# Kernel optimization log

Measured on AMD Instinct MI355X. Metric: run time of the kernel, lower is better.

## Reference

```python
import math
import jax, jax.numpy as jnp
import numpy as np

B, TQ, TK, D = 2, 512, 8192, 1024
N_HEAD, HEAD_DIM = 16, 64
NA = 4096


def setup_inputs() -> dict:
    key = jax.random.key(0)
    ks = jax.random.split(key, 12)
    w = lambda k, shp: (jax.random.normal(k, shp, dtype=jnp.float32) * 0.02)
    return {
        "q": jax.random.normal(ks[0], (B, TQ, D), dtype=jnp.float32),
        "kv": jax.random.normal(ks[1], (B, TK, D), dtype=jnp.float32),
        "Wq": w(ks[2], (D, D)), "bq": jnp.zeros((D,), jnp.float32),
        "Wk": w(ks[3], (D, D)), "bk": jnp.zeros((D,), jnp.float32),
        "Wv": w(ks[4], (D, D)), "bv": jnp.zeros((D,), jnp.float32),
        "Wo": w(ks[5], (D, D)), "bo": jnp.zeros((D,), jnp.float32),
        "active_bias": w(ks[6], (1, D)),
        "inactive_bias": w(ks[7], (1, D)),
        "log_temp": jnp.zeros((), jnp.float32),  # log(temp=1.0)
        "n_actives": NA,
    }


def _attn(qh, kh, vh):
    # qh already carries the full score scale; plain softmax attention
    scores = jnp.einsum("bhqd,bhkd->bhqk", qh, kh)
    w = jax.nn.softmax(scores, axis=-1)
    return jnp.einsum("bhqk,bhkd->bhqd", w, vh)


def reference(q, kv, Wq, bq, Wk, bk, Wv, bv, Wo, bo, active_bias, inactive_bias, log_temp, n_actives):
    Na = int(n_actives)
    Tk = kv.shape[1]
    Ni = Tk - Na

    qp = jnp.einsum("btd,od->bto", q, Wq) + bq
    # group-specific additive biases on kv before K/V projection
    kvb = jnp.concatenate([kv[:, :Na] + active_bias, kv[:, Na:] + inactive_bias], axis=1)
    kp = jnp.einsum("btd,od->bto", kvb, Wk) + bk
    vp = jnp.einsum("btd,od->bto", kvb, Wv) + bv

    # [B, H, T, hd]
    qh = qp.reshape(B, TQ, N_HEAD, HEAD_DIM).transpose(0, 2, 1, 3)
    kh = kp.reshape(B, Tk, N_HEAD, HEAD_DIM).transpose(0, 2, 1, 3)
    vh = vp.reshape(B, Tk, N_HEAD, HEAD_DIM).transpose(0, 2, 1, 3)

    temp = jnp.clip(jnp.exp(log_temp), 0.1, 10.0)
    # torch: q *= 1/sqrt(d); sdpa(q/temp, ...) applies another 1/sqrt(d)
    qs = qh / (jnp.float32(HEAD_DIM) * temp)

    out = jnp.zeros_like(qh)
    if Na > 0:
        out = out + _attn(qs, kh[:, :, :Na], vh[:, :, :Na]) / math.sqrt(max(Na, 1))
    if Ni > 0:
        out = out - _attn(qs, kh[:, :, Na:], vh[:, :, Na:]) / math.sqrt(max(Ni, 1))

    out = out.transpose(0, 2, 1, 3).reshape(B, TQ, D)
    return jnp.einsum("btd,od->bto", out, Wo) + bo
```

## Files before the change

kernel.cpp:

```cpp
#include <hip/hip_runtime.h>
#include <math.h>
#include <stdint.h>

#define B_   2
#define TQ_  512
#define TK_  8192
#define D_   1024
#define NH_  16
#define HD_  64

#define NEG_BIG (-3.0e38f)
#define ASPLIT 8
#define LOG2E 1.4426950408889634f
#define EXP2F(x) __builtin_exp2f(x)

typedef __attribute__((ext_vector_type(8))) short short8;
typedef __attribute__((ext_vector_type(4))) float f32x4;

__device__ __forceinline__ unsigned short f2bf(float x) {
    unsigned u = __float_as_uint(x);
    unsigned r = u + 0x7FFFu + ((u >> 16) & 1u);
    return (unsigned short)(r >> 16);
}
__device__ __forceinline__ float bf2f(unsigned short h) {
    return __uint_as_float(((unsigned)h) << 16);
}
__device__ __forceinline__ short8 pack_bf16x8(float4 lo, float4 hi) {
    union { short8 v; unsigned u[4]; } P;
    asm("v_cvt_pk_bf16_f32 %0, %1, %2" : "=v"(P.u[0]) : "v"(lo.x), "v"(lo.y));
    asm("v_cvt_pk_bf16_f32 %0, %1, %2" : "=v"(P.u[1]) : "v"(lo.z), "v"(lo.w));
    asm("v_cvt_pk_bf16_f32 %0, %1, %2" : "=v"(P.u[2]) : "v"(hi.x), "v"(hi.y));
    asm("v_cvt_pk_bf16_f32 %0, %1, %2" : "=v"(P.u[3]) : "v"(hi.z), "v"(hi.w));
    return P.v;
}

#define GLD16(gp, lp)                                                              \
    __builtin_amdgcn_global_load_lds(                                              \
        (const __attribute__((address_space(1))) unsigned int*)(gp),               \
        (__attribute__((address_space(3))) unsigned int*)(lp), 16, 0, 0)

__global__ __launch_bounds__(256)
void split_w4(const float* __restrict__ W0, const float* __restrict__ W1,
              const float* __restrict__ W2, const float* __restrict__ W3,
              unsigned short* __restrict__ O0, unsigned short* __restrict__ O1,
              unsigned short* __restrict__ O2, unsigned short* __restrict__ O3)
{
    const float* W; unsigned short* O;
    switch (blockIdx.y) {
        case 0:  W = W0; O = O0; break;
        case 1:  W = W1; O = O1; break;
        case 2:  W = W2; O = O2; break;
        default: W = W3; O = O3; break;
    }
    size_t i = ((size_t)blockIdx.x * 256 + threadIdx.x) * 8;
    float4 x0 = *(const float4*)(W + i);
    float4 x1 = *(const float4*)(W + i + 4);
    float a[8] = {x0.x, x0.y, x0.z, x0.w, x1.x, x1.y, x1.z, x1.w};
    union { short8 v; unsigned short u[8]; } H;
#pragma unroll
    for (int j = 0; j < 8; ++j) H.u[j] = f2bf(a[j]);
    *(short8*)(O + i) = H.v;
}

__global__ __launch_bounds__(256)
void split_w(const float* __restrict__ W, unsigned short* __restrict__ Wh)
{
    size_t i = ((size_t)blockIdx.x * 256 + threadIdx.x) * 8;
    float4 x0 = *(const float4*)(W + i);
    float4 x1 = *(const float4*)(W + i + 4);
    float a[8] = {x0.x, x0.y, x0.z, x0.w, x1.x, x1.y, x1.z, x1.w};
    union { short8 v; unsigned short u[8]; } H;
#pragma unroll
    for (int j = 0; j < 8; ++j) H.u[j] = f2bf(a[j]);
    *(short8*)(Wh + i) = H.v;
}

__global__ __launch_bounds__(256)
void bias_gemv(const float* __restrict__ Wk, const float* __restrict__ Wv,
               const float* __restrict__ ab, const float* __restrict__ ib,
               float* __restrict__ gvK, float* __restrict__ gvV)
{
    const int comb = blockIdx.y;
    const float* W = (comb < 2) ? Wk : Wv;
    const float* g = (comb & 1) ? ib : ab;
    float* out = ((comb < 2) ? gvK : gvV) + (comb & 1) * D_;
    const int n = blockIdx.x * 256 + threadIdx.x;
    const float* wr = W + (size_t)n * D_;
    float acc = 0.f;
    for (int d = 0; d < D_; d += 4) {
        float4 w4 = *(const float4*)(wr + d);
        float4 g4 = *(const float4*)(g + d);
        acc += w4.x * g4.x + w4.y * g4.y + w4.z * g4.z + w4.w * g4.w;
    }
    out[n] = acc;
}

__global__ __launch_bounds__(256)
void sdpca_gemm_q(const unsigned short* __restrict__ A, const unsigned short* __restrict__ W,
                  const float* __restrict__ bias, const float* __restrict__ log_temp,
                  unsigned short* __restrict__ Qb)
{
    __shared__ unsigned short AT[128 * 32];
    __shared__ unsigned short BT[128 * 32];
    const int tid  = threadIdx.x;
    const int lane = tid & 63;
    const int w    = tid >> 6;
    const int brow = blockIdx.y * 128;
    const int bcol = blockIdx.x * 128;
    const int wr = w >> 1, wc = w & 1;

    const int   srow = lane >> 2;
    const int   scol = (((lane & 3) ^ ((lane >> 3) & 3)) * 8);
    const size_t gA0 = (size_t)(brow + w * 32 + srow) * D_ + scol;
    const size_t gA1 = gA0 + (size_t)16 * D_;
    const size_t gB0 = (size_t)(bcol + w * 32 + srow) * D_ + scol;
    const size_t gB1 = gB0 + (size_t)16 * D_;
    const int   l0   = (w * 32 +  0) * 32;
    const int   l1   = (w * 32 + 16) * 32;

    f32x4 acc[4][4];
#pragma unroll
    for (int m = 0; m < 4; ++m)
#pragma unroll
        for (int n = 0; n < 4; ++n) acc[m][n] = (f32x4){0.f, 0.f, 0.f, 0.f};

    const int frow = lane & 15;
    const int fko  = (((lane >> 4) ^ ((frow >> 1) & 3)) * 8);

    for (int k0 = 0; k0 < D_; k0 += 32) {
        GLD16(A + gA0 + k0, &AT[l0]);
        GLD16(A + gA1 + k0, &AT[l1]);
        GLD16(W + gB0 + k0, &BT[l0]);
        GLD16(W + gB1 + k0, &BT[l1]);
        __syncthreads();
        short8 bf[4];
#pragma unroll
        for (int n = 0; n < 4; ++n)
            bf[n] = *(const short8*)&BT[(wc * 64 + n * 16 + frow) * 32 + fko];
#pragma unroll
        for (int m = 0; m < 4; ++m) {
            short8 a = *(const short8*)&AT[(wr * 64 + m * 16 + frow) * 32 + fko];
#pragma unroll
            for (int n = 0; n < 4; ++n)
                acc[m][n] = __builtin_amdgcn_mfma_f32_16x16x32_bf16(a, bf[n], acc[m][n], 0, 0, 0);
        }
        __syncthreads();
    }

    float lt    = *log_temp;
    float temp  = fminf(fmaxf(expf(lt), 0.1f), 10.0f);
    float scale = LOG2E / (64.0f * temp);

#pragma unroll
    for (int n = 0; n < 4; ++n) {
        int col = bcol + wc * 64 + n * 16 + frow;
        float bsv = bias[col];
#pragma unroll
        for (int m = 0; m < 4; ++m) {
            int rbase = brow + wr * 64 + m * 16 + (lane >> 4) * 4;
#pragma unroll
            for (int r = 0; r < 4; ++r)
                Qb[(size_t)(rbase + r) * D_ + col] = f2bf((acc[m][n][r] + bsv) * scale);
        }
    }
}

__global__ __launch_bounds__(256)
void sdpca_gemm_kv_fused(const float* __restrict__ kv,
                         const unsigned short* __restrict__ Whk,
                         const unsigned short* __restrict__ Whv,
                         const float* __restrict__ bk, const float* __restrict__ bv,
                         const float* __restrict__ gvK, const float* __restrict__ gvV,
                         const int* __restrict__ nactp,
                         unsigned short* __restrict__ Kb, unsigned short* __restrict__ Vt)
{
    __shared__ unsigned short AT[128 * 32];
    __shared__ unsigned short BT[128 * 32];

    const int tid  = threadIdx.x;
    const int lane = tid & 63;
    const int w    = tid >> 6;
    const int bid  = blockIdx.x;
    const int lid  = (bid & 7) * 128 + (bid >> 3);
    const int brow = (lid >> 3) * 128;
    const int bcol = (lid & 7) * 128;
    const int z    = blockIdx.y;
    const int Na   = *nactp;

    const unsigned short* Wh = z ? Whv : Whk;
    const float* bias        = z ? bv  : bk;
    const float* gv          = z ? gvV : gvK;

    const int wr = w >> 1, wc = w & 1;

    const int srow = lane >> 2;
    const int cg   = lane & 3;
    const int cs   = cg ^ ((srow >> 1) & 3);
    const size_t gA0 = (size_t)(brow + w * 32 + srow) * D_ + cg * 8;
    const size_t gA1 = gA0 + (size_t)16 * D_;
    const size_t gB0 = (size_t)(bcol + w * 32 + srow) * D_ + cg * 8;
    const size_t gB1 = gB0 + (size_t)16 * D_;
    const int    la0 = (w * 32 + srow) * 32 + cs * 8;
    const int    la1 = (w * 32 + 16 + srow) * 32 + cs * 8;

    f32x4 acc[4][4];
#pragma unroll
    for (int m = 0; m < 4; ++m)
#pragma unroll
        for (int n = 0; n < 4; ++n) acc[m][n] = (f32x4){0.f, 0.f, 0.f, 0.f};

    const int frow = lane & 15;
    const int fko  = (((lane >> 4) ^ ((frow >> 1) & 3)) * 8);

    float4 a00 = *(const float4*)(kv + gA0);
    float4 a01 = *(const float4*)(kv + gA0 + 4);
    float4 a10 = *(const float4*)(kv + gA1);
    float4 a11 = *(const float4*)(kv + gA1 + 4);
    short8 br0 = *(const short8*)(Wh + gB0);
    short8 br1 = *(const short8*)(Wh + gB1);

    for (int k0 = 0; k0 < D_; k0 += 32) {
        __syncthreads();
        *(short8*)&AT[la0] = pack_bf16x8(a00, a01);
        *(short8*)&AT[la1] = pack_bf16x8(a10, a11);
        *(short8*)&BT[la0] = br0;
        *(short8*)&BT[la1] = br1;
        __syncthreads();

        if (k0 + 32 < D_) {
            a00 = *(const float4*)(kv + gA0 + k0 + 36 - 4);
            a01 = *(const float4*)(kv + gA0 + k0 + 36);
            a10 = *(const float4*)(kv + gA1 + k0 + 32);
            a11 = *(const float4*)(kv + gA1 + k0 + 36);
            br0 = *(const short8*)(Wh + gB0 + k0 + 32);
            br1 = *(const short8*)(Wh + gB1 + k0 + 32);
        }

        short8 bf[4];
#pragma unroll
        for (int n = 0; n < 4; ++n)
            bf[n] = *(const short8*)&BT[(wc * 64 + n * 16 + frow) * 32 + fko];
#pragma unroll
        for (int m = 0; m < 4; ++m) {
            short8 a = *(const short8*)&AT[(wr * 64 + m * 16 + frow) * 32 + fko];
#pragma unroll
            for (int n = 0; n < 4; ++n)
                acc[m][n] = __builtin_amdgcn_mfma_f32_16x16x32_bf16(a, bf[n], acc[m][n], 0, 0, 0);
        }
    }

    if (z == 0) {
#pragma unroll
        for (int n = 0; n < 4; ++n) {
            int col = bcol + wc * 64 + n * 16 + frow;
            float bsv = bias[col];
            float g0  = gv[col], g1 = gv[D_ + col];
#pragma unroll
            for (int m = 0; m < 4; ++m) {
                int rbase = brow + wr * 64 + m * 16 + (lane >> 4) * 4;
#pragma unroll
                for (int r = 0; r < 4; ++r) {
                    int tok = (rbase + r) & (TK_ - 1);
                    float gval = (tok < Na) ? g0 : g1;
                    Kb[(size_t)(rbase + r) * D_ + col] = f2bf(acc[m][n][r] + bsv + gval);
                }
            }
        }
    } else {
#pragma unroll
        for (int n = 0; n < 4; ++n) {
            int col = bcol + wc * 64 + n * 16 + frow;
            int h   = col >> 6, d = col & 63;
            float bsv = bias[col];
            float g0  = gv[col], g1 = gv[D_ + col];
#pragma unroll
            for (int m = 0; m < 4; ++m) {
                int rbase = brow + wr * 64 + m * 16 + (lane >> 4) * 4;
                int b     = rbase >> 13;
                int tok   = rbase & (TK_ - 1);
                ushort4 o;
                o.x = f2bf(acc[m][n][0] + bsv + ((tok + 0 < Na) ? g0 : g1));
                o.y = f2bf(acc[m][n][1] + bsv + ((tok + 1 < Na) ? g0 : g1));
                o.z = f2bf(acc[m][n][2] + bsv + ((tok + 2 < Na) ? g0 : g1));
                o.w = f2bf(acc[m][n][3] + bsv + ((tok + 3 < Na) ? g0 : g1));
                *(ushort4*)&Vt[((size_t)(b * 16 + h) * 64 + d) * TK_ + tok] = o;
            }
        }
    }
}

template<bool FULL>
__device__ __forceinline__ void attn_pass(
    const f32x4 st[4], int jb, int lo, int hi,
    f32x4& lacc, f32x4 o[4],
    unsigned short* Ps, const unsigned short* Vs,
    int frow, int g, int w)
{
    const int q = w * 16 + frow;
    const short8 kOnes = {(short)0x3F80, (short)0x3F80, (short)0x3F80, (short)0x3F80,
                          (short)0x3F80, (short)0x3F80, (short)0x3F80, (short)0x3F80};
    float p[4][4];
#pragma unroll
    for (int mt = 0; mt < 4; ++mt)
#pragma unroll
        for (int r = 0; r < 4; ++r) {
            float pv = EXP2F(st[mt][r]);
            if (!FULL) {
                int key = jb + mt * 16 + g * 4 + r;
                if (key < lo || key >= hi) pv = 0.f;
            }
            p[mt][r] = pv;
        }

#pragma unroll
    for (int mt = 0; mt < 4; ++mt) {
        unsigned u0, u1;
        asm("v_cvt_pk_bf16_f32 %0, %1, %2" : "=v"(u0) : "v"(p[mt][0]), "v"(p[mt][1]));
        asm("v_cvt_pk_bf16_f32 %0, %1, %2" : "=v"(u1) : "v"(p[mt][2]), "v"(p[mt][3]));
        unsigned* dst = (unsigned*)((char*)Ps + q * 144 + (mt * 16 + g * 4) * 2);
        dst[0] = u0; dst[1] = u1;
    }
    __builtin_amdgcn_sched_barrier(0);

    short8 pb[2];
#pragma unroll
    for (int ks = 0; ks < 2; ++ks)
        pb[ks] = *(const short8*)((const char*)Ps + q * 144 + ks * 64 + g * 16);
    __builtin_amdgcn_s_setprio(1);
#pragma unroll
    for (int mt = 0; mt < 4; ++mt) {
        int row = mt * 16 + frow;
        int rs  = (row & 7) << 4;
#pragma unroll
        for (int ks = 0; ks < 2; ++ks) {
            short8 a = *(const short8*)((const char*)Vs + row * 128 + ((ks * 64 + g * 16) ^ rs));
            o[mt] = __builtin_amdgcn_mfma_f32_16x16x32_bf16(a, pb[ks], o[mt], 0, 0, 0);
        }
    }
#pragma unroll
    for (int ks = 0; ks < 2; ++ks)
        lacc = __builtin_amdgcn_mfma_f32_16x16x32_bf16(kOnes, pb[ks], lacc, 0, 0, 0);
    __builtin_amdgcn_s_setprio(0);
}

__global__ __launch_bounds__(256)
void sdpca_attn_mfma(const unsigned short* __restrict__ Qb,
                     const unsigned short* __restrict__ Kb,
                     const unsigned short* __restrict__ Vt,
                     const int* __restrict__ nactp,
                     unsigned short* __restrict__ pO, float* __restrict__ pL)
{
    __shared__ char smem[25600];
    unsigned short* Ks = (unsigned short*)smem;
    unsigned short* Vs = (unsigned short*)(smem + 8192);
    unsigned short* Ps = (unsigned short*)(smem + 16384);
    float*          Ot = (float*)smem;

    const int tid  = threadIdx.x;
    const int l    = tid & 63, w = tid >> 6;
    const int frow = l & 15,  g = l >> 4;

    const int bid = blockIdx.x;
    const int lid = (bid & 7) * 256 + (bid >> 3);
    const int q0  = (lid & 7) * 64;
    const int bh  = (lid >> 3) & 31;
    const int s   = lid >> 8;
    const int b   = bh >> 4, h = bh & 15;

    const int Na   = *nactp;
    const int ks0  = s * (TK_ / ASPLIT);
    const int nt   = TK_ / ASPLIT / 64;

    short8 qf0, qf1;
    {
        const unsigned short* qp = Qb + (size_t)(b * TQ_ + q0 + w * 16 + frow) * D_ + h * HD_;
        qf0 = *(const short8*)(qp + g * 8);
        qf1 = *(const short8*)(qp + 32 + g * 8);
    }

    f32x4 lA4 = (f32x4){0.f, 0.f, 0.f, 0.f};
    f32x4 lI4 = (f32x4){0.f, 0.f, 0.f, 0.f};
    f32x4 oA[4], oI[4];
#pragma unroll
    for (int mt = 0; mt < 4; ++mt) {
        oA[mt] = (f32x4){0.f, 0.f, 0.f, 0.f};
        oI[mt] = (f32x4){0.f, 0.f, 0.f, 0.f};
    }

    const int srow = tid >> 2;
    const int scb  = (tid & 3) * 32;
    const unsigned short* kg = Kb + (size_t)(b * TK_ + ks0 + srow) * D_ + h * HD_ + (tid & 3) * 16;
    const unsigned short* vg = Vt + ((size_t)bh * HD_ + srow) * TK_ + ks0 + (tid & 3) * 16;
    const int kswz0 = srow * 128 + ((scb +  0) ^ ((srow & 7) << 4));
    const int kswz1 = srow * 128 + ((scb + 16) ^ ((srow & 7) << 4));

    short8 kr0 = *(const short8*)(kg);
    short8 kr1 = *(const short8*)(kg + 8);
    short8 vr0 = *(const short8*)(vg);
    short8 vr1 = *(const short8*)(vg + 8);
    kg += (size_t)64 * D_;
    vg += 64;

    for (int t = 0; t < nt; ++t) {
        const int jb = ks0 + t * 64;
        __syncthreads();
        *(short8*)((char*)Ks + kswz0) = kr0;
        *(short8*)((char*)Ks + kswz1) = kr1;
        *(short8*)((char*)Vs + kswz0) = vr0;
        *(short8*)((char*)Vs + kswz1) = vr1;
        __syncthreads();

        if (t + 1 < nt) {
            kr0 = *(const short8*)(kg);
            kr1 = *(const short8*)(kg + 8);
            vr0 = *(const short8*)(vg);
            vr1 = *(const short8*)(vg + 8);
            kg += (size_t)64 * D_;
            vg += 64;
        }

        f32x4 st[4];
        __builtin_amdgcn_s_setprio(1);
#pragma unroll
        for (int mt = 0; mt < 4; ++mt) {
            int row = mt * 16 + frow;
            int rs  = (row & 7) << 4;
            short8 a0 = *(const short8*)((const char*)Ks + row * 128 + ((g * 16) ^ rs));
            short8 a1 = *(const short8*)((const char*)Ks + row * 128 + ((64 + g * 16) ^ rs));
            f32x4 acc = (f32x4){0.f, 0.f, 0.f, 0.f};
            acc = __builtin_amdgcn_mfma_f32_16x16x32_bf16(a0, qf0, acc, 0, 0, 0);
            acc = __builtin_amdgcn_mfma_f32_16x16x32_bf16(a1, qf1, acc, 0, 0, 0);
            st[mt] = acc;
        }
        __builtin_amdgcn_s_setprio(0);

        const bool hasA = (jb < Na);
        const bool hasI = (jb + 64 > Na);
        if (hasA) {
            if (jb + 64 <= Na) attn_pass<true >(st, jb, 0, Na, lA4, oA, Ps, Vs, frow, g, w);
            else               attn_pass<false>(st, jb, 0, Na, lA4, oA, Ps, Vs, frow, g, w);
        }
        if (hasI) {
            if (jb >= Na)      attn_pass<true >(st, jb, Na, TK_, lI4, oI, Ps, Vs, frow, g, w);
            else               attn_pass<false>(st, jb, Na, TK_, lI4, oI, Ps, Vs, frow, g, w);
        }
    }

    const int q = w * 16 + frow;
#pragma unroll
    for (int grp = 0; grp < 2; ++grp) {
        __syncthreads();
        const f32x4* o = grp ? oI : oA;
#pragma unroll
        for (int mt = 0; mt < 4; ++mt)
            *(f32x4*)&Ot[q * 68 + mt * 16 + g * 4] = o[mt];
        if (g == 0) {
            size_t base = ((size_t)((s * 2 + grp) * (B_ * NH_) + bh)) * TQ_ + q0 + q;
            pL[base] = grp ? lI4[0] : lA4[0];
        }
        __syncthreads();
        {
            int qr = tid >> 2, dc = (tid & 3) * 16;
            size_t rowbase = ((size_t)((s * 2 + grp) * (B_ * NH_) + bh)) * TQ_ + q0 + qr;
            unsigned short* dst = pO + rowbase * HD_ + dc;
            union { short8 v; unsigned short u[8]; } o0, o1;
#pragma unroll
            for (int j = 0; j < 8; ++j) {
                o0.u[j] = f2bf(Ot[qr * 68 + dc + j]);
                o1.u[j] = f2bf(Ot[qr * 68 + dc + 8 + j]);
            }
            *(short8*)(dst)     = o0.v;
            *(short8*)(dst + 8) = o1.v;
        }
    }
}

__global__ __launch_bounds__(256)
void sdpca_combine(const unsigned short* __restrict__ pO, const float* __restrict__ pL,
                   const int* __restrict__ nactp, unsigned short* __restrict__ Aob)
{
    int idx = blockIdx.x * 256 + threadIdx.x;
    int d   = idx & (HD_ - 1);
    int q   = (idx >> 6) & (TQ_ - 1);
    int bh  = idx >> 15;
    int b   = bh >> 4, h = bh & 15;
    int Na  = *nactp;
    int Ni  = TK_ - Na;

    float res = 0.f;
#pragma unroll
    for (int gg = 0; gg < 2; ++gg) {
        float L = 0.f, O = 0.f;
#pragma unroll
        for (int ss = 0; ss < ASPLIT; ++ss) {
            size_t ii = ((size_t)((ss * 2 + gg) * (B_ * NH_) + bh)) * TQ_ + q;
            L += pL[ii];
            O += bf2f(pO[ii * HD_ + d]);
        }
        float r   = (L > 0.f) ? (O / L) : 0.f;
        int   cnt = (gg == 0) ? Na : Ni;
        float sc  = (cnt > 0) ? rsqrtf((float)cnt) : 0.f;
        res += (gg == 0) ? (sc * r) : (-sc * r);
    }
    Aob[((size_t)(b * TQ_ + q)) * D_ + h * HD_ + d] = f2bf(res);
}

__global__ __launch_bounds__(256)
void sdpca_gemm_o(const unsigned short* __restrict__ A, const unsigned short* __restrict__ W,
                  const float* __restrict__ bias, float* __restrict__ C)
{
    __shared__ unsigned short AT[128 * 32];
    __shared__ unsigned short BT[128 * 32];
    const int tid  = threadIdx.x;
    const int lane = tid & 63;
    const int w    = tid >> 6;
    const int brow = blockIdx.y * 128;
    const int bcol = blockIdx.x * 128;
    const int wr = w >> 1, wc = w & 1;

    const int   srow = lane >> 2;
    const int   scol = (((lane & 3) ^ ((lane >> 3) & 3)) * 8);
    const size_t gA0 = (size_t)(brow + w * 32 + srow) * D_ + scol;
    const size_t gA1 = gA0 + (size_t)16 * D_;
    const size_t gB0 = (size_t)(bcol + w * 32 + srow) * D_ + scol;
    const size_t gB1 = gB0 + (size_t)16 * D_;
    const int   l0   = (w * 32 +  0) * 32;
    const int   l1   = (w * 32 + 16) * 32;

    f32x4 acc[4][4];
#pragma unroll
    for (int m = 0; m < 4; ++m)
#pragma unroll
        for (int n = 0; n < 4; ++n) acc[m][n] = (f32x4){0.f, 0.f, 0.f, 0.f};

    const int frow = lane & 15;
    const int fko  = (((lane >> 4) ^ ((frow >> 1) & 3)) * 8);

    for (int k0 = 0; k0 < D_; k0 += 32) {
        GLD16(A + gA0 + k0, &AT[l0]);
        GLD16(A + gA1 + k0, &AT[l1]);
        GLD16(W + gB0 + k0, &BT[l0]);
        GLD16(W + gB1 + k0, &BT[l1]);
        __syncthreads();
        short8 bf[4];
#pragma unroll
        for (int n = 0; n < 4; ++n)
            bf[n] = *(const short8*)&BT[(wc * 64 + n * 16 + frow) * 32 + fko];
#pragma unroll
        for (int m = 0; m < 4; ++m) {
            short8 a = *(const short8*)&AT[(wr * 64 + m * 16 + frow) * 32 + fko];
#pragma unroll
            for (int n = 0; n < 4; ++n)
                acc[m][n] = __builtin_amdgcn_mfma_f32_16x16x32_bf16(a, bf[n], acc[m][n], 0, 0, 0);
        }
        __syncthreads();
    }

#pragma unroll
    for (int n = 0; n < 4; ++n) {
        int col = bcol + wc * 64 + n * 16 + frow;
        float bsv = bias[col];
#pragma unroll
        for (int m = 0; m < 4; ++m) {
            int rbase = brow + wr * 64 + m * 16 + (lane >> 4) * 4;
#pragma unroll
            for (int r = 0; r < 4; ++r)
                C[(size_t)(rbase + r) * D_ + col] = acc[m][n][r] + bsv;
        }
    }
}

extern "C" void kernel_launch(void* const* d_in, const int* in_sizes, int n_in,
                              void* d_out, int out_size, void* d_ws, size_t ws_size,
                              hipStream_t stream) {
    (void)in_sizes; (void)n_in; (void)out_size; (void)ws_size;
    const float* q   = (const float*)d_in[0];
    const float* kv  = (const float*)d_in[1];
    const float* Wq  = (const float*)d_in[2];
    const float* bq  = (const float*)d_in[3];
    const float* Wk  = (const float*)d_in[4];
    const float* bk  = (const float*)d_in[5];
    const float* Wv  = (const float*)d_in[6];
    const float* bv  = (const float*)d_in[7];
    const float* Wo  = (const float*)d_in[8];
    const float* bo  = (const float*)d_in[9];
    const float* ab  = (const float*)d_in[10];
    const float* ib  = (const float*)d_in[11];
    const float* lt  = (const float*)d_in[12];
    const int*   na  = (const int*)d_in[13];

    char* ws = (char*)d_ws;
    const size_t nQ  = (size_t)B_ * TQ_ * D_;
    const size_t nKV = (size_t)B_ * TK_ * D_;
    const size_t nW  = (size_t)D_ * D_;
    const size_t nML = (size_t)ASPLIT * 2 * B_ * NH_ * TQ_;

    float*          gvK = (float*)ws;
    float*          gvV = gvK + 2 * D_;
    unsigned short* Whk = (unsigned short*)(gvV + 2 * D_);
    unsigned short* Whv = Whk + nW;
    unsigned short* Kb  = Whv + nW;
    unsigned short* Vt  = Kb + nKV;
    unsigned short* Qb  = Vt + nKV;
    unsigned short* qbb = Qb + nQ;
    unsigned short* Wqb = qbb + nQ;
    unsigned short* Wob = Wqb + nW;
    unsigned short* Aob = Wob + nW;
    float* pL = (float*)(Aob + nQ);
    unsigned short* pO = (unsigned short*)(pL + nML);

    dim3 blk(256);
    split_w            <<<dim3((int)(nQ / 8 / 256)),  blk, 0, stream>>>(q,  qbb);
    split_w4           <<<dim3((int)(nW / 8 / 256), 4), blk, 0, stream>>>(
        Wq, Wo, Wk, Wv, Wqb, Wob, Whk, Whv);
    bias_gemv          <<<dim3(4, 4),                 blk, 0, stream>>>(Wk, Wv, ab, ib, gvK, gvV);
    sdpca_gemm_q       <<<dim3(8, 8),                 blk, 0, stream>>>(qbb, Wqb, bq, lt, Qb);
    sdpca_gemm_kv_fused<<<dim3(1024, 2),              blk, 0, stream>>>(
        kv, Whk, Whv, bk, bv, gvK, gvV, na, Kb, Vt);
    sdpca_attn_mfma    <<<dim3(2048),                 blk, 0, stream>>>(Qb, Kb, Vt, na, pO, pL);
    sdpca_combine      <<<dim3((B_ * TQ_ * D_) / 256), blk, 0, stream>>>(pO, pL, na, Aob);
    sdpca_gemm_o       <<<dim3(8, 8),                 blk, 0, stream>>>(Aob, Wob, bo, (float*)d_out);
}
```

Baseline: 257.1 us.

## Stream fp32 kv tiles directly to LDS and merge q cast into weight split

The KV projection GEMM now loads fp32 kv tiles straight into shared memory with global_load_lds using an XOR-swizzled layout, converting to bf16 only when forming MFMA fragments. The weight tiles are also loaded via global_load_lds, replacing the register prefetch plus LDS store path. The separate q-to-bf16 cast kernel is folded into the weight split kernel as a fifth grid slice, which works because nQ equals nW here. In exchange the fp32 A tile doubles LDS use, there is no register-level prefetch overlap, and every wave repeats the bf16 pack work inside the inner loop.

```diff
diff --git a/kernel.cpp b/kernel.cpp
--- a/kernel.cpp
+++ b/kernel.cpp
@@ -25,12 +25,12 @@
 __device__ __forceinline__ float bf2f(unsigned short h) {
     return __uint_as_float(((unsigned)h) << 16);
 }
-__device__ __forceinline__ short8 pack_bf16x8(float4 lo, float4 hi) {
+__device__ __forceinline__ short8 pack_bf16x8(f32x4 lo, f32x4 hi) {
     union { short8 v; unsigned u[4]; } P;
-    asm("v_cvt_pk_bf16_f32 %0, %1, %2" : "=v"(P.u[0]) : "v"(lo.x), "v"(lo.y));
-    asm("v_cvt_pk_bf16_f32 %0, %1, %2" : "=v"(P.u[1]) : "v"(lo.z), "v"(lo.w));
-    asm("v_cvt_pk_bf16_f32 %0, %1, %2" : "=v"(P.u[2]) : "v"(hi.x), "v"(hi.y));
-    asm("v_cvt_pk_bf16_f32 %0, %1, %2" : "=v"(P.u[3]) : "v"(hi.z), "v"(hi.w));
+    asm("v_cvt_pk_bf16_f32 %0, %1, %2" : "=v"(P.u[0]) : "v"(lo[0]), "v"(lo[1]));
+    asm("v_cvt_pk_bf16_f32 %0, %1, %2" : "=v"(P.u[1]) : "v"(lo[2]), "v"(lo[3]));
+    asm("v_cvt_pk_bf16_f32 %0, %1, %2" : "=v"(P.u[2]) : "v"(hi[0]), "v"(hi[1]));
+    asm("v_cvt_pk_bf16_f32 %0, %1, %2" : "=v"(P.u[3]) : "v"(hi[2]), "v"(hi[3]));
     return P.v;
 }
 
@@ -40,17 +40,20 @@
         (__attribute__((address_space(3))) unsigned int*)(lp), 16, 0, 0)
 
 __global__ __launch_bounds__(256)
-void split_w4(const float* __restrict__ W0, const float* __restrict__ W1,
+void split_w5(const float* __restrict__ W0, const float* __restrict__ W1,
               const float* __restrict__ W2, const float* __restrict__ W3,
+              const float* __restrict__ W4,
               unsigned short* __restrict__ O0, unsigned short* __restrict__ O1,
-              unsigned short* __restrict__ O2, unsigned short* __restrict__ O3)
+              unsigned short* __restrict__ O2, unsigned short* __restrict__ O3,
+              unsigned short* __restrict__ O4)
 {
     const float* W; unsigned short* O;
     switch (blockIdx.y) {
         case 0:  W = W0; O = O0; break;
         case 1:  W = W1; O = O1; break;
         case 2:  W = W2; O = O2; break;
-        default: W = W3; O = O3; break;
+        case 3:  W = W3; O = O3; break;
+        default: W = W4; O = O4; break;
     }
     size_t i = ((size_t)blockIdx.x * 256 + threadIdx.x) * 8;
     float4 x0 = *(const float4*)(W + i);
@@ -60,19 +63,6 @@
 #pragma unroll
     for (int j = 0; j < 8; ++j) H.u[j] = f2bf(a[j]);
     *(short8*)(O + i) = H.v;
-}
-
-__global__ __launch_bounds__(256)
-void split_w(const float* __restrict__ W, unsigned short* __restrict__ Wh)
-{
-    size_t i = ((size_t)blockIdx.x * 256 + threadIdx.x) * 8;
-    float4 x0 = *(const float4*)(W + i);
-    float4 x1 = *(const float4*)(W + i + 4);
-    float a[8] = {x0.x, x0.y, x0.z, x0.w, x1.x, x1.y, x1.z, x1.w};
-    union { short8 v; unsigned short u[8]; } H;
-#pragma unroll
-    for (int j = 0; j < 8; ++j) H.u[j] = f2bf(a[j]);
-    *(short8*)(Wh + i) = H.v;
 }
 
 __global__ __launch_bounds__(256)
@@ -174,8 +164,8 @@
                          const int* __restrict__ nactp,
                          unsigned short* __restrict__ Kb, unsigned short* __restrict__ Vt)
 {
-    __shared__ unsigned short AT[128 * 32];
-    __shared__ unsigned short BT[128 * 32];
+    __shared__ float          ATf[128 * 32];
+    __shared__ unsigned short BT [128 * 32];
 
     const int tid  = threadIdx.x;
     const int lane = tid & 63;
@@ -193,15 +183,16 @@
 
     const int wr = w >> 1, wc = w & 1;
 
-    const int srow = lane >> 2;
-    const int cg   = lane & 3;
-    const int cs   = cg ^ ((srow >> 1) & 3);
-    const size_t gA0 = (size_t)(brow + w * 32 + srow) * D_ + cg * 8;
-    const size_t gA1 = gA0 + (size_t)16 * D_;
-    const size_t gB0 = (size_t)(bcol + w * 32 + srow) * D_ + cg * 8;
-    const size_t gB1 = gB0 + (size_t)16 * D_;
-    const int    la0 = (w * 32 + srow) * 32 + cs * 8;
-    const int    la1 = (w * 32 + 16 + srow) * 32 + cs * 8;
+    const int    arow = lane >> 3;
+    const int    acs  = (lane & 7) ^ arow;
+    const size_t gAr  = (size_t)(brow + w * 32 + arow) * D_ + acs * 4;
+
+    const int    srow = lane >> 2;
+    const int    scol = (((lane & 3) ^ ((lane >> 3) & 3)) * 8);
+    const size_t gB0  = (size_t)(bcol + w * 32 + srow) * D_ + scol;
+    const size_t gB1  = gB0 + (size_t)16 * D_;
+    const int    lB0  = (w * 32 +  0) * 32;
+    const int    lB1  = (w * 32 + 16) * 32;
 
     f32x4 acc[4][4];
 #pragma unroll
@@ -210,43 +201,34 @@
         for (int n = 0; n < 4; ++n) acc[m][n] = (f32x4){0.f, 0.f, 0.f, 0.f};
 
     const int frow = lane & 15;
-    const int fko  = (((lane >> 4) ^ ((frow >> 1) & 3)) * 8);
-
-    float4 a00 = *(const float4*)(kv + gA0);
-    float4 a01 = *(const float4*)(kv + gA0 + 4);
-    float4 a10 = *(const float4*)(kv + gA1);
-    float4 a11 = *(const float4*)(kv + gA1 + 4);
-    short8 br0 = *(const short8*)(Wh + gB0);
-    short8 br1 = *(const short8*)(Wh + gB1);
+    const int ko   = lane >> 4;
+    const int fkoB = ((ko ^ ((frow >> 1) & 3)) * 8);
 
     for (int k0 = 0; k0 < D_; k0 += 32) {
-        __syncthreads();
-        *(short8*)&AT[la0] = pack_bf16x8(a00, a01);
-        *(short8*)&AT[la1] = pack_bf16x8(a10, a11);
-        *(short8*)&BT[la0] = br0;
-        *(short8*)&BT[la1] = br1;
-        __syncthreads();
-
-        if (k0 + 32 < D_) {
-            a00 = *(const float4*)(kv + gA0 + k0 + 36 - 4);
-            a01 = *(const float4*)(kv + gA0 + k0 + 36);
-            a10 = *(const float4*)(kv + gA1 + k0 + 32);
-            a11 = *(const float4*)(kv + gA1 + k0 + 36);
-            br0 = *(const short8*)(Wh + gB0 + k0 + 32);
-            br1 = *(const short8*)(Wh + gB1 + k0 + 32);
-        }
+#pragma unroll
+        for (int p = 0; p < 4; ++p)
+            GLD16(kv + gAr + (size_t)(8 * p) * D_ + k0, &ATf[(w * 32 + 8 * p) * 32]);
+        GLD16(Wh + gB0 + k0, &BT[lB0]);
+        GLD16(Wh + gB1 + k0, &BT[lB1]);
+        __syncthreads();
 
         short8 bf[4];
 #pragma unroll
         for (int n = 0; n < 4; ++n)
-            bf[n] = *(const short8*)&BT[(wc * 64 + n * 16 + frow) * 32 + fko];
+            bf[n] = *(const short8*)&BT[(wc * 64 + n * 16 + frow) * 32 + fkoB];
 #pragma unroll
         for (int m = 0; m < 4; ++m) {
-            short8 a = *(const short8*)&AT[(wr * 64 + m * 16 + frow) * 32 + fko];
+            int R  = wr * 64 + m * 16 + frow;
+            int c0 = (2 * ko)     ^ (R & 7);
+            int c1 = (2 * ko + 1) ^ (R & 7);
+            f32x4 f0 = *(const f32x4*)&ATf[R * 32 + c0 * 4];
+            f32x4 f1 = *(const f32x4*)&ATf[R * 32 + c1 * 4];
+            short8 a = pack_bf16x8(f0, f1);
 #pragma unroll
             for (int n = 0; n < 4; ++n)
                 acc[m][n] = __builtin_amdgcn_mfma_f32_16x16x32_bf16(a, bf[n], acc[m][n], 0, 0, 0);
         }
+        __syncthreads();
     }
 
     if (z == 0) {
@@ -261,8 +243,8 @@
 #pragma unroll
                 for (int r = 0; r < 4; ++r) {
                     int tok = (rbase + r) & (TK_ - 1);
-                    float gval = (tok < Na) ? g0 : g1;
-                    Kb[(size_t)(rbase + r) * D_ + col] = f2bf(acc[m][n][r] + bsv + gval);
+                    Kb[(size_t)(rbase + r) * D_ + col] =
+                        f2bf(acc[m][n][r] + bsv + ((tok < Na) ? g0 : g1));
                 }
             }
         }
@@ -610,9 +592,8 @@
     unsigned short* pO = (unsigned short*)(pL + nML);
 
     dim3 blk(256);
-    split_w            <<<dim3((int)(nQ / 8 / 256)),  blk, 0, stream>>>(q,  qbb);
-    split_w4           <<<dim3((int)(nW / 8 / 256), 4), blk, 0, stream>>>(
-        Wq, Wo, Wk, Wv, Wqb, Wob, Whk, Whv);
+    split_w5           <<<dim3((int)(nW / 8 / 256), 5), blk, 0, stream>>>(
+        q, Wq, Wo, Wk, Wv, qbb, Wqb, Wob, Whk, Whv);
     bias_gemv          <<<dim3(4, 4),                 blk, 0, stream>>>(Wk, Wv, ab, ib, gvK, gvV);
     sdpca_gemm_q       <<<dim3(8, 8),                 blk, 0, stream>>>(qbb, Wqb, bq, lt, Qb);
     sdpca_gemm_kv_fused<<<dim3(1024, 2),              blk, 0, stream>>>(
```

After: 276.3 us. +7.5%, slower.
